# Optimization experiments

Measured on AMD Instinct MI355X. Metric: run time of the kernel, lower is better.

Reference implementation:

```python
import jax, jax.numpy as jnp
import numpy as np

N_NODES = 100000
N_EDGES = 1000000
IN_DIM = 128
HID = 128
OUT_DIM = 40


def setup_inputs() -> dict:
    key = jax.random.key(0)
    ks = jax.random.split(key, 16)
    x = jax.random.normal(ks[0], (N_NODES, IN_DIM), dtype=jnp.float32)
    edge_index = jax.random.randint(ks[1], (2, N_EDGES), 0, N_NODES, dtype=jnp.int64)
    s = 0.05
    # GAT layer 1 (in->hid, heads=1, concat=True)
    W1 = jax.random.normal(ks[2], (HID, IN_DIM), jnp.float32) * s
    b1 = jnp.zeros((HID,), jnp.float32)
    att1 = jax.random.normal(ks[3], (1, 2 * HID), jnp.float32) * s
    bias1 = jnp.zeros((HID,), jnp.float32)
    # GAT layer 2 (hid->hid)
    W2 = jax.random.normal(ks[4], (HID, HID), jnp.float32) * s
    b2 = jnp.zeros((HID,), jnp.float32)
    att2 = jax.random.normal(ks[5], (1, 2 * HID), jnp.float32) * s
    bias2 = jnp.zeros((HID,), jnp.float32)
    # post_mp: Linear(hid,hid) -> Dropout -> Linear(hid,out)
    Wp1 = jax.random.normal(ks[6], (HID, HID), jnp.float32) * s
    bp1 = jnp.zeros((HID,), jnp.float32)
    Wp2 = jax.random.normal(ks[7], (OUT_DIM, HID), jnp.float32) * s
    bp2 = jnp.zeros((OUT_DIM,), jnp.float32)
    return dict(x=x, edge_index=edge_index, W1=W1, b1=b1, att1=att1, bias1=bias1,
                W2=W2, b2=b2, att2=att2, bias2=bias2,
                Wp1=Wp1, bp1=bp1, Wp2=Wp2, bp2=bp2)


def gat_layer(x, src, dst, W, b, att, bias, n_nodes):
    # x: [N, Fin] -> h: [N, C] (heads=1, concat=True)
    h = x @ W.T + b
    C = h.shape[1]
    att_i, att_j = att[0, :C], att[0, C:]  # split: first half pairs with x_i (dst), second with x_j (src)
    # per-node scalar projections, then gather per edge (avoids [E,2C] concat)
    e = (h @ att_i)[dst] + (h @ att_j)[src]  # [E]
    e = jnp.where(e > 0, e, 0.2 * e)  # leaky_relu(0.2)
    # segment softmax over destination nodes
    m = jax.ops.segment_max(e, dst, num_segments=n_nodes)
    ex = jnp.exp(e - m[dst])
    denom = jax.ops.segment_sum(ex, dst, num_segments=n_nodes)
    alpha = ex / denom[dst]
    out = jax.ops.segment_sum(h[src] * alpha[:, None], dst, num_segments=n_nodes)
    return out + bias


def reference(x, edge_index, W1, b1, att1, bias1, W2, b2, att2, bias2, Wp1, bp1, Wp2, bp2):
    src, dst = edge_index[0], edge_index[1]
    n = x.shape[0]
    h = jax.nn.relu(gat_layer(x, src, dst, W1, b1, att1, bias1, n))  # dropout p=0 -> identity
    h = jax.nn.relu(gat_layer(h, src, dst, W2, b2, att2, bias2, n))
    y = (h @ Wp1.T + bp1) @ Wp2.T + bp2  # post_mp (eval: dropout identity)
    return jax.nn.log_softmax(y, axis=1)
```

## Files before the change

### kernel.cpp

```cpp
#include <hip/hip_runtime.h>

#define N_NODES 100000
#define N_EDGES 1000000
#define HID 128
#define OUT_DIM 40
#define CSR_W 64
#define CUR_STRIDE 16
#define GEMM_TILES 1563
#define G2_TILES 782
#define PROJ_TILES 1563
#define EDGE_BLK 977
#define WC_BLK 25

typedef __attribute__((ext_vector_type(8))) short bf16x8;
typedef __attribute__((ext_vector_type(8))) unsigned short u16x8;
typedef __attribute__((ext_vector_type(4))) float f32x4;

__device__ inline unsigned short f2bf(float f) {
    unsigned u = __float_as_uint(f);
    u += 0x7fffu + ((u >> 16) & 1u);
    return (unsigned short)(u >> 16);
}
__device__ inline float bf2f(unsigned short u) {
    return __uint_as_float(((unsigned)u) << 16);
}

__device__ inline float4 ld4(const float* p) { return *(const float4*)p; }

__global__ __launch_bounds__(256) void zero_conv_kernel(
    float4* __restrict__ p, int n4,
    const float* __restrict__ W1, const float* __restrict__ W2,
    unsigned short* __restrict__ W1b, unsigned short* __restrict__ W2b)
{
    if (blockIdx.x < 512) {
        int i = blockIdx.x * 256 + threadIdx.x;
        const int stride = 512 * 256;
        float4 z = make_float4(0.f, 0.f, 0.f, 0.f);
        for (; i < n4; i += stride) p[i] = z;
        return;
    }
    const int L = (blockIdx.x - 512) * 256 + threadIdx.x;
    const int e = L * 8;
    const float* s;
    unsigned short* d;
    if (e < HID * HID) { s = W1 + e; d = W1b + e; }
    else               { s = W2 + (e - HID * HID); d = W2b + (e - HID * HID); }
    float4 a = *(const float4*)s;
    float4 b = *(const float4*)(s + 4);
    ushort4 u0, u1;
    u0.x = f2bf(a.x); u0.y = f2bf(a.y); u0.z = f2bf(a.z); u0.w = f2bf(a.w);
    u1.x = f2bf(b.x); u1.y = f2bf(b.y); u1.z = f2bf(b.z); u1.w = f2bf(b.w);
    *(ushort4*)d = u0;
    *(ushort4*)(d + 4) = u1;
}

#define LDA 136
__device__ __forceinline__ void gemm_tile_body_f32(
    int tile, const float* __restrict__ A, const unsigned short* __restrict__ Wb,
    const float* __restrict__ out_bias, const float* __restrict__ att,
    unsigned short* __restrict__ Cb, float* __restrict__ hi, float* __restrict__ hj,
    int n_rows, unsigned short* As, unsigned short* Ws)
{
    const int t = threadIdx.x;
    const int row0 = tile * 64;

    for (int i = 0; i < 8; i++) {
        int lin = t + i * 256;
        int r = lin >> 5;
        int k = (lin & 31) * 4;
        int gr = row0 + r;
        float4 av = make_float4(0.f, 0.f, 0.f, 0.f);
        if (gr < n_rows) av = ld4(A + (size_t)gr * HID + k);
        ushort4 bv;
        bv.x = f2bf(av.x); bv.y = f2bf(av.y); bv.z = f2bf(av.z); bv.w = f2bf(av.w);
        *(ushort4*)(&As[r * LDA + k]) = bv;
    }
    for (int i = 0; i < 8; i++) {
        int lin = t + i * 256;
        int r = lin >> 4;
        int k = (lin & 15) * 8;
        *(bf16x8*)(&Ws[r * LDA + k]) = *(const bf16x8*)(Wb + (size_t)r * HID + k);
    }
    __syncthreads();

    const int wave = t >> 6, lane = t & 63;
    const int lrow = lane & 15, quad = lane >> 4;
    const int wrow = wave * 16;

    f32x4 acc[8];
    #pragma unroll
    for (int ni = 0; ni < 8; ni++) acc[ni] = (f32x4){0.f, 0.f, 0.f, 0.f};

    #pragma unroll
    for (int ks = 0; ks < 4; ks++) {
        const int kb = ks * 32 + quad * 8;
        bf16x8 af = *(bf16x8*)(&As[(wrow + lrow) * LDA + kb]);
        #pragma unroll
        for (int ni = 0; ni < 8; ni++) {
            bf16x8 bfr = *(bf16x8*)(&Ws[(ni * 16 + lrow) * LDA + kb]);
            acc[ni] = __builtin_amdgcn_mfma_f32_16x16x32_bf16(af, bfr, acc[ni], 0, 0, 0);
        }
    }

    float pi[4] = {0.f, 0.f, 0.f, 0.f}, pj[4] = {0.f, 0.f, 0.f, 0.f};
    const int rbase = row0 + wrow + quad * 4;
    #pragma unroll
    for (int ni = 0; ni < 8; ni++) {
        const int col = ni * 16 + lrow;
        const float bo = out_bias[col];
        const float ai = att[col], aj = att[HID + col];
        #pragma unroll
        for (int r = 0; r < 4; r++) {
            float v = acc[ni][r] + bo;
            int gr = rbase + r;
            if (gr < n_rows) Cb[(size_t)gr * HID + col] = f2bf(v);
            pi[r] = fmaf(v, ai, pi[r]);
            pj[r] = fmaf(v, aj, pj[r]);
        }
    }
    #pragma unroll
    for (int o = 1; o < 16; o <<= 1) {
        #pragma unroll
        for (int r = 0; r < 4; r++) {
            pi[r] += __shfl_xor(pi[r], o);
            pj[r] += __shfl_xor(pj[r], o);
        }
    }
    if (lrow == 0) {
        #pragma unroll
        for (int r = 0; r < 4; r++) {
            int gr = rbase + r;
            if (gr < n_rows) { hi[gr] = pi[r]; hj[gr] = pj[r]; }
        }
    }
}

__global__ __launch_bounds__(256) void combined_prep(
    const float* __restrict__ x, const unsigned short* __restrict__ W1b,
    const float* __restrict__ b1, const float* __restrict__ att1,
    const float* __restrict__ Wp1, const float* __restrict__ bp1,
    const float* __restrict__ Wp2, const float* __restrict__ bp2,
    const int* __restrict__ src, const int* __restrict__ dst,
    unsigned* __restrict__ cursor, int* __restrict__ csr,
    unsigned short* __restrict__ hbuf, float* __restrict__ hi, float* __restrict__ hj,
    unsigned short* __restrict__ Wcb, float* __restrict__ bc)
{
    __shared__ unsigned short As[64 * LDA];
    __shared__ unsigned short Ws[128 * LDA];
    const int b = blockIdx.x, g = b >> 3, r = b & 7;

    if (r < 3) {
        const int eid = g * 3 + r;
        if (eid >= EDGE_BLK) return;
        int e = eid * 1024 + threadIdx.x;
        #pragma unroll
        for (int j = 0; j < 4; j++, e += 256) {
            if (e < N_EDGES) {
                int d = dst[e], s = src[e];
                unsigned p = atomicAdd(&cursor[d << 4], 1u);
                if (p < CSR_W) __builtin_nontemporal_store(s, &csr[(d << 6) + p]);
            }
        }
        return;
    }
    const int oid = g * 5 + (r - 3);
    if (oid < WC_BLK) {
        int t = oid * 256 + threadIdx.x;
        if (t < OUT_DIM * HID) {
            int o = t >> 7, k = t & 127;
            float s = 0.f;
            for (int j = 0; j < HID; j++) s = fmaf(Wp2[o * HID + j], Wp1[j * HID + k], s);
            Wcb[t] = f2bf(s);
        } else if (t < 48 * HID) {
            Wcb[t] = 0;
        } else if (t < 48 * HID + OUT_DIM) {
            int o = t - 48 * HID;
            float s = bp2[o];
            for (int j = 0; j < HID; j++) s = fmaf(Wp2[o * HID + j], bp1[j], s);
            bc[o] = s;
        }
        return;
    }
    const int tile = oid - WC_BLK;
    if (tile >= GEMM_TILES) return;
    gemm_tile_body_f32(tile, x, W1b, b1, att1, hbuf, hi, hj, N_NODES, As, Ws);
}

__global__ __launch_bounds__(256) void gemm_mfma_b128(
    const unsigned short* __restrict__ A, const unsigned short* __restrict__ Wb,
    const float* __restrict__ out_bias, const float* __restrict__ att,
    unsigned short* __restrict__ Cb, float* __restrict__ hi, float* __restrict__ hj,
    int n_rows)
{
    __shared__ unsigned short As[128 * LDA];
    __shared__ unsigned short Ws[128 * LDA];
    const int t = threadIdx.x;
    const int row0 = blockIdx.x * 128;

    for (int i = 0; i < 8; i++) {
        int lin = t + i * 256;
        int r = lin >> 4;
        int k = (lin & 15) * 8;
        int gr = row0 + r;
        bf16x8 v = (bf16x8){0, 0, 0, 0, 0, 0, 0, 0};
        if (gr < n_rows) v = *(const bf16x8*)(A + (size_t)gr * HID + k);
        *(bf16x8*)(&As[r * LDA + k]) = v;
    }
    for (int i = 0; i < 8; i++) {
        int lin = t + i * 256;
        int r = lin >> 4;
        int k = (lin & 15) * 8;
        *(bf16x8*)(&Ws[r * LDA + k]) = *(const bf16x8*)(Wb + (size_t)r * HID + k);
    }
    __syncthreads();

    const int wave = t >> 6, lane = t & 63;
    const int lrow = lane & 15, quad = lane >> 4;

    f32x4 acc[2][8];
    #pragma unroll
    for (int mt = 0; mt < 2; mt++)
        #pragma unroll
        for (int ni = 0; ni < 8; ni++) acc[mt][ni] = (f32x4){0.f, 0.f, 0.f, 0.f};

    #pragma unroll
    for (int ks = 0; ks < 4; ks++) {
        const int kb = ks * 32 + quad * 8;
        bf16x8 af0 = *(bf16x8*)(&As[(wave * 32 + lrow) * LDA + kb]);
        bf16x8 af1 = *(bf16x8*)(&As[(wave * 32 + 16 + lrow) * LDA + kb]);
        #pragma unroll
        for (int ni = 0; ni < 8; ni++) {
            bf16x8 bfr = *(bf16x8*)(&Ws[(ni * 16 + lrow) * LDA + kb]);
            acc[0][ni] = __builtin_amdgcn_mfma_f32_16x16x32_bf16(af0, bfr, acc[0][ni], 0, 0, 0);
            acc[1][ni] = __builtin_amdgcn_mfma_f32_16x16x32_bf16(af1, bfr, acc[1][ni], 0, 0, 0);
        }
    }

    #pragma unroll
    for (int mt = 0; mt < 2; mt++) {
        float pi[4] = {0.f, 0.f, 0.f, 0.f}, pj[4] = {0.f, 0.f, 0.f, 0.f};
        const int rbase = row0 + wave * 32 + mt * 16 + quad * 4;
        #pragma unroll
        for (int ni = 0; ni < 8; ni++) {
            const int col = ni * 16 + lrow;
            const float bo = out_bias[col];
            const float ai = att[col], aj = att[HID + col];
            #pragma unroll
            for (int r = 0; r < 4; r++) {
                float v = acc[mt][ni][r] + bo;
                int gr = rbase + r;
                if (gr < n_rows) Cb[(size_t)gr * HID + col] = f2bf(v);
                pi[r] = fmaf(v, ai, pi[r]);
                pj[r] = fmaf(v, aj, pj[r]);
            }
        }
        #pragma unroll
        for (int o = 1; o < 16; o <<= 1) {
            #pragma unroll
            for (int r = 0; r < 4; r++) {
                pi[r] += __shfl_xor(pi[r], o);
                pj[r] += __shfl_xor(pj[r], o);
            }
        }
        if (lrow == 0) {
            #pragma unroll
            for (int r = 0; r < 4; r++) {
                int gr = rbase + r;
                if (gr < n_rows) { hi[gr] = pi[r]; hj[gr] = pj[r]; }
            }
        }
    }
}

__global__ __launch_bounds__(256) void fused_gat(
    const unsigned* __restrict__ cursor, const int* __restrict__ csr,
    const unsigned short* __restrict__ hb,
    const float* __restrict__ hi, const float* __restrict__ hj,
    const float* __restrict__ bias,
    unsigned short* __restrict__ out)
{
    const int wave = threadIdx.x >> 6;
    const int lane = threadIdx.x & 63;
    const int d = blockIdx.x * 4 + wave;
    if (d >= N_NODES) return;
    unsigned deg = cursor[d << 4];
    if (deg > CSR_W) deg = CSR_W;
    const int cnt = (int)deg;
    const float hid = hi[d];
    const int base = d << 6;

    int sv = 0;
    float ev = -INFINITY;
    if (lane < cnt) {
        sv = csr[base + lane];
        float e = hid + hj[sv];
        ev = e > 0.f ? e : 0.2f * e;
    }
    float m = ev;
    #pragma unroll
    for (int o = 32; o; o >>= 1) m = fmaxf(m, __shfl_xor(m, o));
    const float exv = (lane < cnt) ? __expf(ev - m) : 0.f;
    float denom = exv;
    #pragma unroll
    for (int o = 32; o; o >>= 1) denom += __shfl_xor(denom, o);

    const int g = lane >> 4;
    const int co = (lane & 15) * 8;
    float a[8];
    #pragma unroll
    for (int c = 0; c < 8; c++) a[c] = 0.f;

    int i = 0;
    for (; i + 8 <= cnt; i += 8) {
        #pragma unroll
        for (int u = 0; u < 2; u++) {
            const int e = i + u * 4 + g;
            const int s = __shfl(sv, e);
            const float w = __shfl(exv, e);
            const u16x8 q = *(const u16x8*)(hb + (size_t)s * HID + co);
            #pragma unroll
            for (int c = 0; c < 8; c++) a[c] = fmaf(w, bf2f(q[c]), a[c]);
        }
    }
    if (i + 4 <= cnt) {
        const int e = i + g;
        const int s = __shfl(sv, e);
        const float w = __shfl(exv, e);
        const u16x8 q = *(const u16x8*)(hb + (size_t)s * HID + co);
        #pragma unroll
        for (int c = 0; c < 8; c++) a[c] = fmaf(w, bf2f(q[c]), a[c]);
        i += 4;
    }
    if (i < cnt) {
        const int e = i + g;
        const int s = __shfl(sv, e);
        const float w = __shfl(exv, e);
        const u16x8 q = *(const u16x8*)(hb + (size_t)s * HID + co);
        #pragma unroll
        for (int c = 0; c < 8; c++) a[c] = fmaf(w, bf2f(q[c]), a[c]);
    }

    #pragma unroll
    for (int c = 0; c < 8; c++) {
        a[c] += __shfl_xor(a[c], 16);
        a[c] += __shfl_xor(a[c], 32);
    }

    const float inv = cnt ? 1.f / denom : 0.f;
    if (lane < 16) {
        const float4 bv0 = *(const float4*)(bias + co);
        const float4 bv1 = *(const float4*)(bias + co + 4);
        u16x8 o8;
        o8[0] = f2bf(fmaxf(fmaf(a[0], inv, bv0.x), 0.f));
        o8[1] = f2bf(fmaxf(fmaf(a[1], inv, bv0.y), 0.f));
        o8[2] = f2bf(fmaxf(fmaf(a[2], inv, bv0.z), 0.f));
        o8[3] = f2bf(fmaxf(fmaf(a[3], inv, bv0.w), 0.f));
        o8[4] = f2bf(fmaxf(fmaf(a[4], inv, bv1.x), 0.f));
        o8[5] = f2bf(fmaxf(fmaf(a[5], inv, bv1.y), 0.f));
        o8[6] = f2bf(fmaxf(fmaf(a[6], inv, bv1.z), 0.f));
        o8[7] = f2bf(fmaxf(fmaf(a[7], inv, bv1.w), 0.f));
        *(u16x8*)(out + (size_t)d * HID + co) = o8;
    }
}

__global__ __launch_bounds__(256) void final_proj_mfma(
    const unsigned short* __restrict__ agg,
    const unsigned short* __restrict__ Wcb, const float* __restrict__ bc,
    float* __restrict__ out)
{
    __shared__ unsigned short As[64 * LDA];
    __shared__ unsigned short Ws[48 * LDA];
    const int t = threadIdx.x;
    const int node0 = blockIdx.x * 64;

    for (int i = 0; i < 4; i++) {
        int lin = t + i * 256;
        int r = lin >> 4;
        int k = (lin & 15) * 8;
        int gr = node0 + r;
        bf16x8 v = (bf16x8){0, 0, 0, 0, 0, 0, 0, 0};
        if (gr < N_NODES) v = *(const bf16x8*)(agg + (size_t)gr * HID + k);
        *(bf16x8*)(&As[r * LDA + k]) = v;
    }
    for (int i = 0; i < 3; i++) {
        int lin = t + i * 256;
        int r = lin >> 4;
        int k = (lin & 15) * 8;
        *(bf16x8*)(&Ws[r * LDA + k]) = *(const bf16x8*)(Wcb + (size_t)r * HID + k);
    }
    __syncthreads();

    const int wave = t >> 6, lane = t & 63;
    const int lrow = lane & 15, quad = lane >> 4;
    const int wrow = wave * 16;

    f32x4 acc[3];
    #pragma unroll
    for (int nt = 0; nt < 3; nt++) acc[nt] = (f32x4){0.f, 0.f, 0.f, 0.f};

    #pragma unroll
    for (int ks = 0; ks < 4; ks++) {
        const int kb = ks * 32 + quad * 8;
        bf16x8 af = *(bf16x8*)(&As[(wrow + lrow) * LDA + kb]);
        #pragma unroll
        for (int nt = 0; nt < 3; nt++) {
            bf16x8 bfr = *(bf16x8*)(&Ws[(nt * 16 + lrow) * LDA + kb]);
            acc[nt] = __builtin_amdgcn_mfma_f32_16x16x32_bf16(af, bfr, acc[nt], 0, 0, 0);
        }
    }

    int cols[3]; float bcv[3]; bool valid[3];
    #pragma unroll
    for (int nt = 0; nt < 3; nt++) {
        cols[nt] = nt * 16 + lrow;
        valid[nt] = cols[nt] < OUT_DIM;
        bcv[nt] = valid[nt] ? bc[cols[nt]] : 0.f;
    }
    const int rbase = node0 + wrow + quad * 4;
    #pragma unroll
    for (int r = 0; r < 4; r++) {
        float v[3];
        float mx = -INFINITY;
        #pragma unroll
        for (int nt = 0; nt < 3; nt++) {
            v[nt] = acc[nt][r] + bcv[nt];
            if (valid[nt]) mx = fmaxf(mx, v[nt]);
        }
        #pragma unroll
        for (int o = 1; o < 16; o <<= 1) mx = fmaxf(mx, __shfl_xor(mx, o));
        float s = 0.f;
        #pragma unroll
        for (int nt = 0; nt < 3; nt++)
            if (valid[nt]) s += __expf(v[nt] - mx);
        #pragma unroll
        for (int o = 1; o < 16; o <<= 1) s += __shfl_xor(s, o);
        const float lse = mx + __logf(s);
        const int node = rbase + r;
        if (node < N_NODES) {
            #pragma unroll
            for (int nt = 0; nt < 3; nt++)
                if (valid[nt]) out[(size_t)node * OUT_DIM + cols[nt]] = v[nt] - lse;
        }
    }
}

extern "C" void kernel_launch(void* const* d_in, const int* in_sizes, int n_in,
                              void* d_out, int out_size, void* d_ws, size_t ws_size,
                              hipStream_t stream)
{
    const float* x     = (const float*)d_in[0];
    const int*   ei    = (const int*)d_in[1];
    const float* W1    = (const float*)d_in[2];
    const float* b1    = (const float*)d_in[3];
    const float* att1  = (const float*)d_in[4];
    const float* bias1 = (const float*)d_in[5];
    const float* W2    = (const float*)d_in[6];
    const float* b2    = (const float*)d_in[7];
    const float* att2  = (const float*)d_in[8];
    const float* bias2 = (const float*)d_in[9];
    const float* Wp1   = (const float*)d_in[10];
    const float* bp1   = (const float*)d_in[11];
    const float* Wp2   = (const float*)d_in[12];
    const float* bp2   = (const float*)d_in[13];
    float* out = (float*)d_out;

    const int* src = ei;
    const int* dst = ei + N_EDGES;

    char* ws = (char*)d_ws;
    unsigned short* hbuf = (unsigned short*)ws;
    unsigned short* aggb = hbuf + (size_t)N_NODES * HID;
    float* hi      = (float*)(aggb + (size_t)N_NODES * HID);
    float* hj      = hi + N_NODES;
    unsigned* cursor = (unsigned*)(hj + N_NODES);
    int* csr       = (int*)(cursor + (size_t)N_NODES * CUR_STRIDE);
    unsigned short* Wcb = (unsigned short*)(csr + (size_t)N_NODES * CSR_W);
    unsigned short* W1b = Wcb + 48 * HID;
    unsigned short* W2b = W1b + HID * HID;
    float* bc      = (float*)(W2b + HID * HID);

    const int prep_blocks = 326 * 8;

    zero_conv_kernel<<<528, 256, 0, stream>>>(
        (float4*)cursor, N_NODES * CUR_STRIDE / 4, W1, W2, W1b, W2b);

    combined_prep<<<prep_blocks, 256, 0, stream>>>(
        x, W1b, b1, att1, Wp1, bp1, Wp2, bp2, src, dst,
        cursor, csr, hbuf, hi, hj, Wcb, bc);

    fused_gat<<<N_NODES / 4, 256, 0, stream>>>(cursor, csr, hbuf, hi, hj, bias1, aggb);

    gemm_mfma_b128<<<G2_TILES, 256, 0, stream>>>(aggb, W2b, b2, att2, hbuf, hi, hj, N_NODES);
    fused_gat<<<N_NODES / 4, 256, 0, stream>>>(cursor, csr, hbuf, hi, hj, bias2, aggb);

    final_proj_mfma<<<PROJ_TILES, 256, 0, stream>>>(aggb, Wcb, bc, out);
}
```

Baseline: 305.7 us.

## Fuse second GAT aggregation with final projection and log-softmax

Merges the layer-2 GAT aggregation kernel with the final projection and log-softmax into one kernel. Each wave aggregates one node, then multiplies the result by the combined 40x128 post-MP weights held in LDS using scalar FMAs and shuffle reductions. This removes a kernel launch and the write and re-read of the bf16 aggregated activations, at the cost of extra shuffle-heavy ALU work per node in place of MFMA. It also switches the CSR scatter from nontemporal stores to plain stores.

Measured after the change: 353.7 us. 1.16x slower.

```diff
diff --git a/kernel.cpp b/kernel.cpp
--- a/kernel.cpp
+++ b/kernel.cpp
@@ -8,7 +8,6 @@
 #define CUR_STRIDE 16
 #define GEMM_TILES 1563
 #define G2_TILES 782
-#define PROJ_TILES 1563
 #define EDGE_BLK 977
 #define WC_BLK 25
 
@@ -158,7 +157,7 @@
             if (e < N_EDGES) {
                 int d = dst[e], s = src[e];
                 unsigned p = atomicAdd(&cursor[d << 4], 1u);
-                if (p < CSR_W) __builtin_nontemporal_store(s, &csr[(d << 6) + p]);
+                if (p < CSR_W) csr[(d << 6) + p] = s;
             }
         }
         return;
@@ -363,84 +362,138 @@
     }
 }
 
-__global__ __launch_bounds__(256) void final_proj_mfma(
-    const unsigned short* __restrict__ agg,
+__global__ __launch_bounds__(256) void fused_gat_proj(
+    const unsigned* __restrict__ cursor, const int* __restrict__ csr,
+    const unsigned short* __restrict__ hb,
+    const float* __restrict__ hi, const float* __restrict__ hj,
+    const float* __restrict__ bias,
     const unsigned short* __restrict__ Wcb, const float* __restrict__ bc,
     float* __restrict__ out)
 {
-    __shared__ unsigned short As[64 * LDA];
-    __shared__ unsigned short Ws[48 * LDA];
+    __shared__ unsigned short Wcs[40 * LDA];
     const int t = threadIdx.x;
-    const int node0 = blockIdx.x * 64;
-
-    for (int i = 0; i < 4; i++) {
-        int lin = t + i * 256;
-        int r = lin >> 4;
-        int k = (lin & 15) * 8;
-        int gr = node0 + r;
-        bf16x8 v = (bf16x8){0, 0, 0, 0, 0, 0, 0, 0};
-        if (gr < N_NODES) v = *(const bf16x8*)(agg + (size_t)gr * HID + k);
-        *(bf16x8*)(&As[r * LDA + k]) = v;
-    }
+    #pragma unroll
     for (int i = 0; i < 3; i++) {
         int lin = t + i * 256;
-        int r = lin >> 4;
-        int k = (lin & 15) * 8;
-        *(bf16x8*)(&Ws[r * LDA + k]) = *(const bf16x8*)(Wcb + (size_t)r * HID + k);
+        if (lin < 640) {
+            int r = lin >> 4;
+            int k = (lin & 15) * 8;
+            *(bf16x8*)(&Wcs[r * LDA + k]) = *(const bf16x8*)(Wcb + (size_t)r * HID + k);
+        }
     }
     __syncthreads();
 
-    const int wave = t >> 6, lane = t & 63;
-    const int lrow = lane & 15, quad = lane >> 4;
-    const int wrow = wave * 16;
-
-    f32x4 acc[3];
-    #pragma unroll
-    for (int nt = 0; nt < 3; nt++) acc[nt] = (f32x4){0.f, 0.f, 0.f, 0.f};
-
-    #pragma unroll
-    for (int ks = 0; ks < 4; ks++) {
-        const int kb = ks * 32 + quad * 8;
-        bf16x8 af = *(bf16x8*)(&As[(wrow + lrow) * LDA + kb]);
-        #pragma unroll
-        for (int nt = 0; nt < 3; nt++) {
-            bf16x8 bfr = *(bf16x8*)(&Ws[(nt * 16 + lrow) * LDA + kb]);
-            acc[nt] = __builtin_amdgcn_mfma_f32_16x16x32_bf16(af, bfr, acc[nt], 0, 0, 0);
-        }
-    }
-
-    int cols[3]; float bcv[3]; bool valid[3];
-    #pragma unroll
-    for (int nt = 0; nt < 3; nt++) {
-        cols[nt] = nt * 16 + lrow;
-        valid[nt] = cols[nt] < OUT_DIM;
-        bcv[nt] = valid[nt] ? bc[cols[nt]] : 0.f;
-    }
-    const int rbase = node0 + wrow + quad * 4;
-    #pragma unroll
-    for (int r = 0; r < 4; r++) {
-        float v[3];
-        float mx = -INFINITY;
-        #pragma unroll
-        for (int nt = 0; nt < 3; nt++) {
-            v[nt] = acc[nt][r] + bcv[nt];
-            if (valid[nt]) mx = fmaxf(mx, v[nt]);
-        }
-        #pragma unroll
-        for (int o = 1; o < 16; o <<= 1) mx = fmaxf(mx, __shfl_xor(mx, o));
-        float s = 0.f;
-        #pragma unroll
-        for (int nt = 0; nt < 3; nt++)
-            if (valid[nt]) s += __expf(v[nt] - mx);
-        #pragma unroll
-        for (int o = 1; o < 16; o <<= 1) s += __shfl_xor(s, o);
-        const float lse = mx + __logf(s);
-        const int node = rbase + r;
-        if (node < N_NODES) {
+    const int wave = t >> 6;
+    const int lane = t & 63;
+    const int d = blockIdx.x * 4 + wave;
+    if (d >= N_NODES) return;
+    unsigned deg = cursor[d << 4];
+    if (deg > CSR_W) deg = CSR_W;
+    const int cnt = (int)deg;
+    const float hid = hi[d];
+    const int base = d << 6;
+
+    int sv = 0;
+    float ev = -INFINITY;
+    if (lane < cnt) {
+        sv = csr[base + lane];
+        float e = hid + hj[sv];
+        ev = e > 0.f ? e : 0.2f * e;
+    }
+    float m = ev;
+    #pragma unroll
+    for (int o = 32; o; o >>= 1) m = fmaxf(m, __shfl_xor(m, o));
+    const float exv = (lane < cnt) ? __expf(ev - m) : 0.f;
+    float denom = exv;
+    #pragma unroll
+    for (int o = 32; o; o >>= 1) denom += __shfl_xor(denom, o);
+
+    const int g = lane >> 4;
+    const int co = (lane & 15) * 8;
+    float a[8];
+    #pragma unroll
+    for (int c = 0; c < 8; c++) a[c] = 0.f;
+
+    int i = 0;
+    for (; i + 8 <= cnt; i += 8) {
+        #pragma unroll
+        for (int u = 0; u < 2; u++) {
+            const int e = i + u * 4 + g;
+            const int s = __shfl(sv, e);
+            const float w = __shfl(exv, e);
+            const u16x8 q = *(const u16x8*)(hb + (size_t)s * HID + co);
             #pragma unroll
-            for (int nt = 0; nt < 3; nt++)
-                if (valid[nt]) out[(size_t)node * OUT_DIM + cols[nt]] = v[nt] - lse;
-        }
+            for (int c = 0; c < 8; c++) a[c] = fmaf(w, bf2f(q[c]), a[c]);
+        }
+    }
+    if (i + 4 <= cnt) {
+        const int e = i + g;
+        const int s = __shfl(sv, e);
+        const float w = __shfl(exv, e);
+        const u16x8 q = *(const u16x8*)(hb + (size_t)s * HID + co);
+        #pragma unroll
+        for (int c = 0; c < 8; c++) a[c] = fmaf(w, bf2f(q[c]), a[c]);
+        i += 4;
+    }
+    if (i < cnt) {
+        const int e = i + g;
+        const int s = __shfl(sv, e);
+        const float w = __shfl(exv, e);
+        const u16x8 q = *(const u16x8*)(hb + (size_t)s * HID + co);
+        #pragma unroll
+        for (int c = 0; c < 8; c++) a[c] = fmaf(w, bf2f(q[c]), a[c]);
+    }
+
+    #pragma unroll
+    for (int c = 0; c < 8; c++) {
+        a[c] += __shfl_xor(a[c], 16);
+        a[c] += __shfl_xor(a[c], 32);
+    }
+
+    const float inv = cnt ? 1.f / denom : 0.f;
+    const float4 bv0 = *(const float4*)(bias + co);
+    const float4 bv1 = *(const float4*)(bias + co + 4);
+    float rr[8];
+    rr[0] = fmaxf(fmaf(a[0], inv, bv0.x), 0.f);
+    rr[1] = fmaxf(fmaf(a[1], inv, bv0.y), 0.f);
+    rr[2] = fmaxf(fmaf(a[2], inv, bv0.z), 0.f);
+    rr[3] = fmaxf(fmaf(a[3], inv, bv0.w), 0.f);
+    rr[4] = fmaxf(fmaf(a[4], inv, bv1.x), 0.f);
+    rr[5] = fmaxf(fmaf(a[5], inv, bv1.y), 0.f);
+    rr[6] = fmaxf(fmaf(a[6], inv, bv1.z), 0.f);
+    rr[7] = fmaxf(fmaf(a[7], inv, bv1.w), 0.f);
+
+    const int g10 = g * 10;
+    float y[10];
+    #pragma unroll
+    for (int u = 0; u < 10; u++) {
+        const int og = g10 + u;
+        const bf16x8 wv = *(const bf16x8*)(&Wcs[og * LDA + co]);
+        float p = 0.f;
+        #pragma unroll
+        for (int c = 0; c < 8; c++)
+            p = fmaf(rr[c], bf2f((unsigned short)wv[c]), p);
+        #pragma unroll
+        for (int o = 1; o < 16; o <<= 1) p += __shfl_xor(p, o);
+        y[u] = p + bc[og];
+    }
+
+    float mx = y[0];
+    #pragma unroll
+    for (int u = 1; u < 10; u++) mx = fmaxf(mx, y[u]);
+    mx = fmaxf(mx, __shfl_xor(mx, 16));
+    mx = fmaxf(mx, __shfl_xor(mx, 32));
+    float s = 0.f;
+    #pragma unroll
+    for (int u = 0; u < 10; u++) s += __expf(y[u] - mx);
+    s += __shfl_xor(s, 16);
+    s += __shfl_xor(s, 32);
+    const float lse = mx + __logf(s);
+
+    if ((lane & 15) == 0) {
+        float* op = out + (size_t)d * OUT_DIM + g10;
+        #pragma unroll
+        for (int u = 0; u < 10; u++) op[u] = y[u] - lse;
     }
 }
 
@@ -491,7 +544,7 @@
     fused_gat<<<N_NODES / 4, 256, 0, stream>>>(cursor, csr, hbuf, hi, hj, bias1, aggb);
 
     gemm_mfma_b128<<<G2_TILES, 256, 0, stream>>>(aggb, W2b, b2, att2, hbuf, hi, hj, N_NODES);
-    fused_gat<<<N_NODES / 4, 256, 0, stream>>>(cursor, csr, hbuf, hi, hj, bias2, aggb);
-
-    final_proj_mfma<<<PROJ_TILES, 256, 0, stream>>>(aggb, Wcb, bc, out);
-}
+
+    fused_gat_proj<<<N_NODES / 4, 256, 0, stream>>>(
+        cursor, csr, hbuf, hi, hj, bias2, Wcb, bc, out);
+}
```

## Process two GEMM tiles per block and enlarge final projection tile

Applied to the files above, without the earlier changes.

In the combined prep kernel, each GEMM block now loads W1 into shared memory once and processes two 64-row tiles, so fewer blocks repeat the weight load. The edge/GEMM block interleave ratio shifts to 4:4 and the grid shrinks to match. The CSR store becomes a regular store instead of a nontemporal one. The final projection kernel uses 128-row tiles with two M-subtiles per wave, halving its block count and reusing B fragments. The trade-off is less parallelism per kernel and a different cache behaviour for the CSR writes.

After: 333.0 us. 1.09x slower.

```diff
diff --git a/kernel.cpp b/kernel.cpp
--- a/kernel.cpp
+++ b/kernel.cpp
@@ -7,8 +7,9 @@
 #define CSR_W 64
 #define CUR_STRIDE 16
 #define GEMM_TILES 1563
+#define GEMM_BLKS 782
 #define G2_TILES 782
-#define PROJ_TILES 1563
+#define PROJ_TILES 782
 #define EDGE_BLK 977
 #define WC_BLK 25
 
@@ -55,11 +56,11 @@
 }
 
 #define LDA 136
-__device__ __forceinline__ void gemm_tile_body_f32(
-    int tile, const float* __restrict__ A, const unsigned short* __restrict__ Wb,
+__device__ __forceinline__ void gemm1_tile(
+    int tile, const float* __restrict__ A,
     const float* __restrict__ out_bias, const float* __restrict__ att,
     unsigned short* __restrict__ Cb, float* __restrict__ hi, float* __restrict__ hj,
-    int n_rows, unsigned short* As, unsigned short* Ws)
+    unsigned short* As, unsigned short* Ws)
 {
     const int t = threadIdx.x;
     const int row0 = tile * 64;
@@ -70,16 +71,10 @@
         int k = (lin & 31) * 4;
         int gr = row0 + r;
         float4 av = make_float4(0.f, 0.f, 0.f, 0.f);
-        if (gr < n_rows) av = ld4(A + (size_t)gr * HID + k);
+        if (gr < N_NODES) av = ld4(A + (size_t)gr * HID + k);
         ushort4 bv;
         bv.x = f2bf(av.x); bv.y = f2bf(av.y); bv.z = f2bf(av.z); bv.w = f2bf(av.w);
         *(ushort4*)(&As[r * LDA + k]) = bv;
-    }
-    for (int i = 0; i < 8; i++) {
-        int lin = t + i * 256;
-        int r = lin >> 4;
-        int k = (lin & 15) * 8;
-        *(bf16x8*)(&Ws[r * LDA + k]) = *(const bf16x8*)(Wb + (size_t)r * HID + k);
     }
     __syncthreads();
 
@@ -113,7 +108,7 @@
         for (int r = 0; r < 4; r++) {
             float v = acc[ni][r] + bo;
             int gr = rbase + r;
-            if (gr < n_rows) Cb[(size_t)gr * HID + col] = f2bf(v);
+            if (gr < N_NODES) Cb[(size_t)gr * HID + col] = f2bf(v);
             pi[r] = fmaf(v, ai, pi[r]);
             pj[r] = fmaf(v, aj, pj[r]);
         }
@@ -130,9 +125,10 @@
         #pragma unroll
         for (int r = 0; r < 4; r++) {
             int gr = rbase + r;
-            if (gr < n_rows) { hi[gr] = pi[r]; hj[gr] = pj[r]; }
-        }
-    }
+            if (gr < N_NODES) { hi[gr] = pi[r]; hj[gr] = pj[r]; }
+        }
+    }
+    __syncthreads();
 }
 
 __global__ __launch_bounds__(256) void combined_prep(
@@ -149,8 +145,8 @@
     __shared__ unsigned short Ws[128 * LDA];
     const int b = blockIdx.x, g = b >> 3, r = b & 7;
 
-    if (r < 3) {
-        const int eid = g * 3 + r;
+    if (r < 4) {
+        const int eid = g * 4 + r;
         if (eid >= EDGE_BLK) return;
         int e = eid * 1024 + threadIdx.x;
         #pragma unroll
@@ -158,12 +154,12 @@
             if (e < N_EDGES) {
                 int d = dst[e], s = src[e];
                 unsigned p = atomicAdd(&cursor[d << 4], 1u);
-                if (p < CSR_W) __builtin_nontemporal_store(s, &csr[(d << 6) + p]);
+                if (p < CSR_W) csr[(d << 6) + p] = s;
             }
         }
         return;
     }
-    const int oid = g * 5 + (r - 3);
+    const int oid = g * 4 + (r - 4);
     if (oid < WC_BLK) {
         int t = oid * 256 + threadIdx.x;
         if (t < OUT_DIM * HID) {
@@ -181,9 +177,22 @@
         }
         return;
     }
-    const int tile = oid - WC_BLK;
-    if (tile >= GEMM_TILES) return;
-    gemm_tile_body_f32(tile, x, W1b, b1, att1, hbuf, hi, hj, N_NODES, As, Ws);
+    const int gb = oid - WC_BLK;
+    if (gb >= GEMM_BLKS) return;
+
+    {
+        const int t = threadIdx.x;
+        for (int i = 0; i < 8; i++) {
+            int lin = t + i * 256;
+            int rr = lin >> 4;
+            int k = (lin & 15) * 8;
+            *(bf16x8*)(&Ws[rr * LDA + k]) = *(const bf16x8*)(W1b + (size_t)rr * HID + k);
+        }
+    }
+    const int tile0 = gb * 2;
+    gemm1_tile(tile0, x, b1, att1, hbuf, hi, hj, As, Ws);
+    if (tile0 + 1 < GEMM_TILES)
+        gemm1_tile(tile0 + 1, x, b1, att1, hbuf, hi, hj, As, Ws);
 }
 
 __global__ __launch_bounds__(256) void gemm_mfma_b128(
@@ -368,12 +377,12 @@
     const unsigned short* __restrict__ Wcb, const float* __restrict__ bc,
     float* __restrict__ out)
 {
-    __shared__ unsigned short As[64 * LDA];
+    __shared__ unsigned short As[128 * LDA];
     __shared__ unsigned short Ws[48 * LDA];
     const int t = threadIdx.x;
-    const int node0 = blockIdx.x * 64;
-
-    for (int i = 0; i < 4; i++) {
+    const int node0 = blockIdx.x * 128;
+
+    for (int i = 0; i < 8; i++) {
         int lin = t + i * 256;
         int r = lin >> 4;
         int k = (lin & 15) * 8;
@@ -392,20 +401,23 @@
 
     const int wave = t >> 6, lane = t & 63;
     const int lrow = lane & 15, quad = lane >> 4;
-    const int wrow = wave * 16;
-
-    f32x4 acc[3];
-    #pragma unroll
-    for (int nt = 0; nt < 3; nt++) acc[nt] = (f32x4){0.f, 0.f, 0.f, 0.f};
+
+    f32x4 acc[2][3];
+    #pragma unroll
+    for (int mt = 0; mt < 2; mt++)
+        #pragma unroll
+        for (int nt = 0; nt < 3; nt++) acc[mt][nt] = (f32x4){0.f, 0.f, 0.f, 0.f};
 
     #pragma unroll
     for (int ks = 0; ks < 4; ks++) {
         const int kb = ks * 32 + quad * 8;
-        bf16x8 af = *(bf16x8*)(&As[(wrow + lrow) * LDA + kb]);
+        bf16x8 af0 = *(bf16x8*)(&As[(wave * 32 + lrow) * LDA + kb]);
+        bf16x8 af1 = *(bf16x8*)(&As[(wave * 32 + 16 + lrow) * LDA + kb]);
         #pragma unroll
         for (int nt = 0; nt < 3; nt++) {
             bf16x8 bfr = *(bf16x8*)(&Ws[(nt * 16 + lrow) * LDA + kb]);
-            acc[nt] = __builtin_amdgcn_mfma_f32_16x16x32_bf16(af, bfr, acc[nt], 0, 0, 0);
+            acc[0][nt] = __builtin_amdgcn_mfma_f32_16x16x32_bf16(af0, bfr, acc[0][nt], 0, 0, 0);
+            acc[1][nt] = __builtin_amdgcn_mfma_f32_16x16x32_bf16(af1, bfr, acc[1][nt], 0, 0, 0);
         }
     }
 
@@ -416,30 +428,33 @@
         valid[nt] = cols[nt] < OUT_DIM;
         bcv[nt] = valid[nt] ? bc[cols[nt]] : 0.f;
     }
-    const int rbase = node0 + wrow + quad * 4;
-    #pragma unroll
-    for (int r = 0; r < 4; r++) {
-        float v[3];
-        float mx = -INFINITY;
-        #pragma unroll
-        for (int nt = 0; nt < 3; nt++) {
-            v[nt] = acc[nt][r] + bcv[nt];
-            if (valid[nt]) mx = fmaxf(mx, v[nt]);
-        }
-        #pragma unroll
-        for (int o = 1; o < 16; o <<= 1) mx = fmaxf(mx, __shfl_xor(mx, o));
-        float s = 0.f;
-        #pragma unroll
-        for (int nt = 0; nt < 3; nt++)
-            if (valid[nt]) s += __expf(v[nt] - mx);
-        #pragma unroll
-        for (int o = 1; o < 16; o <<= 1) s += __shfl_xor(s, o);
-        const float lse = mx + __logf(s);
-        const int node = rbase + r;
-        if (node < N_NODES) {
+    #pragma unroll
+    for (int mt = 0; mt < 2; mt++) {
+        const int rbase = node0 + wave * 32 + mt * 16 + quad * 4;
+        #pragma unroll
+        for (int r = 0; r < 4; r++) {
+            float v[3];
+            float mx = -INFINITY;
+            #pragma unroll
+            for (int nt = 0; nt < 3; nt++) {
+                v[nt] = acc[mt][nt][r] + bcv[nt];
+                if (valid[nt]) mx = fmaxf(mx, v[nt]);
+            }
+            #pragma unroll
+            for (int o = 1; o < 16; o <<= 1) mx = fmaxf(mx, __shfl_xor(mx, o));
+            float s = 0.f;
             #pragma unroll
             for (int nt = 0; nt < 3; nt++)
-                if (valid[nt]) out[(size_t)node * OUT_DIM + cols[nt]] = v[nt] - lse;
+                if (valid[nt]) s += __expf(v[nt] - mx);
+            #pragma unroll
+            for (int o = 1; o < 16; o <<= 1) s += __shfl_xor(s, o);
+            const float lse = mx + __logf(s);
+            const int node = rbase + r;
+            if (node < N_NODES) {
+                #pragma unroll
+                for (int nt = 0; nt < 3; nt++)
+                    if (valid[nt]) out[(size_t)node * OUT_DIM + cols[nt]] = v[nt] - lse;
+            }
         }
     }
 }
@@ -479,7 +494,7 @@
     unsigned short* W2b = W1b + HID * HID;
     float* bc      = (float*)(W2b + HID * HID);
 
-    const int prep_blocks = 326 * 8;
+    const int prep_blocks = 245 * 8;
 
     zero_conv_kernel<<<528, 256, 0, stream>>>(
         (float4*)cursor, N_NODES * CUR_STRIDE / 4, W1, W2, W1b, W2b);
```
